# Optimization experiments

Hardware: AMD Instinct MI355X
Metric: run time of the kernel (lower is better)

## Reference

```python
import jax, jax.numpy as jnp
import numpy as np

EPS = 1e-05
HEAD_DIM = 32


def setup_inputs() -> dict:
    key = jax.random.key(0)
    ks = jax.random.split(key, 8)
    b, c, h, w = 8, 512, 64, 64
    s = 1.0 / np.sqrt(c).astype(np.float32)
    return {
        "q": jax.random.normal(ks[0], (b, c, h, w), jnp.float32),
        "k": jax.random.normal(ks[1], (b, c, h, w), jnp.float32),
        "v": jax.random.normal(ks[2], (b, c, h, w), jnp.float32),
        "Wq": jax.random.normal(ks[3], (c, c), jnp.float32) * s,
        "Wk": jax.random.normal(ks[4], (c, c), jnp.float32) * s,
        "Wv": jax.random.normal(ks[5], (c, c), jnp.float32) * s,
        "Wp": jax.random.normal(ks[6], (c, c), jnp.float32) * s,
        "bp": jax.random.normal(ks[7], (c,), jnp.float32) * 0.02,
    }


def reference(q, k, v, Wq, Wk, Wv, Wp, bp):
    b, c, h, w = q.shape
    n = h * w
    hd = HEAD_DIM
    nh = c // hd

    def proj_heads(x, W):
        # NCHW -> (b, n, c) tokens, then Linear (x @ W.T), then split heads
        t = x.reshape(b, c, n).transpose(0, 2, 1)          # (b, n, c)
        y = jnp.einsum('bnc,dc->bnd', t, W)                # torch Linear: x @ W.T
        return y.reshape(b, n, nh, hd)                     # (b, n, h, d)

    # elu feature map: elu(x) + 1
    Q = jax.nn.elu(proj_heads(q, Wq)) + 1.0
    K = jax.nn.elu(proj_heads(k, Wk)) + 1.0
    V = proj_heads(v, Wv)

    # NOTE: faithful to original einsums — KV contracts over HEADS per token,
    # Z uses K summed over the sequence.
    KV = jnp.einsum('bnhd,bnhm->bnmd', K, V)               # (b, n, d_out=m? -> (b,n,hd,hd))
    Z = 1.0 / (jnp.einsum('bnhd,bhd->bnh', Q, K.sum(axis=1)) + EPS)  # (b, n, h)
    out = jnp.einsum('bnhd,bnmd,bnh->bnhm', Q, KV, Z)      # (b, n, h, m)

    out = out.reshape(b, n, c)                             # merge heads
    out = jnp.einsum('bnc,dc->bnd', out, Wp) + bp          # output projection
    return out.transpose(0, 2, 1).reshape(b, c, h, w)
```

## Files before the change

### kernel.cpp

```cpp
#include <hip/hip_runtime.h>
#include <hip/hip_bf16.h>

#define BATCH 8
#define CD 512
#define NT 4096
#define EPSV 1e-5f

using u16x8 = __attribute__((ext_vector_type(8))) unsigned short;
using u16x4 = __attribute__((ext_vector_type(4))) unsigned short;
using bf8   = __attribute__((ext_vector_type(8))) short;
using f32x4 = __attribute__((ext_vector_type(4))) float;

__device__ __forceinline__ float b2f(unsigned short u) {
    union { unsigned int i; float f; } x; x.i = ((unsigned int)u) << 16; return x.f;
}
__device__ __forceinline__ unsigned short f2b(float f) {
    unsigned int x = __float_as_uint(f);
    unsigned int r = (x + 0x7fffu + ((x >> 16) & 1u)) >> 16;
    return (unsigned short)r;
}
__device__ __forceinline__ unsigned int cvtpk(float a, float b) {
    unsigned int r;
    asm("v_cvt_pk_bf16_f32 %0, %1, %2" : "=v"(r) : "v"(a), "v"(b));
    return r;
}
__device__ __forceinline__ void gload_lds16(const void* g, void* l) {
    __builtin_amdgcn_global_load_lds((const __attribute__((address_space(1))) unsigned int*)g,
                                     (__attribute__((address_space(3))) unsigned int*)l, 16, 0, 0);
}
__device__ __forceinline__ int swz8(int r) { return (r ^ (r >> 3)) & 7; }

__global__ __launch_bounds__(256)
void wconv(const float* __restrict__ W0, const float* __restrict__ W1,
           const float* __restrict__ W2, const float* __restrict__ W3,
           unsigned short* __restrict__ Wb) {
    const float* src = (blockIdx.y == 0) ? W0 : (blockIdx.y == 1) ? W1 : (blockIdx.y == 2) ? W2 : W3;
    unsigned short* dst = Wb + (size_t)blockIdx.y * CD * CD;
    const int base = blockIdx.x * 4096 + threadIdx.x * 16;
    u16x8 o0, o1;
    #pragma unroll
    for (int i = 0; i < 4; ++i) {
        float4 v = *reinterpret_cast<const float4*>(src + base + i * 4);
        unsigned short* t = (i < 2) ? (unsigned short*)&o0 : (unsigned short*)&o1;
        t[(i & 1) * 4 + 0] = f2b(v.x); t[(i & 1) * 4 + 1] = f2b(v.y);
        t[(i & 1) * 4 + 2] = f2b(v.z); t[(i & 1) * 4 + 3] = f2b(v.w);
    }
    *(u16x8*)(dst + base)     = o0;
    *(u16x8*)(dst + base + 8) = o1;
}

__global__ __launch_bounds__(256)
void proj_gemm_all(const float* __restrict__ q, const float* __restrict__ k,
                   const float* __restrict__ v, const unsigned short* __restrict__ Wb,
                   unsigned short* __restrict__ Qp, unsigned short* __restrict__ Kp,
                   unsigned short* __restrict__ Vp, float* __restrict__ Kpart) {
    __shared__ __align__(16) unsigned short Xs[64 * 512];
    __shared__ __align__(16) unsigned short Ws[128 * 64];
    const int nper = gridDim.x >> 3;
    const int work = (blockIdx.x & 7) * nper + (blockIdx.x >> 3);
    const int mat  = work / 512;
    const int rem  = work - mat * 512;
    const int b    = rem >> 6;
    const int tile = rem & 63;
    const int n0   = tile * 64;
    const float* Xb = (mat == 0 ? q : mat == 1 ? k : v) + (size_t)b * CD * NT;
    const unsigned short* W = Wb + (size_t)mat * CD * CD;
    unsigned short* Tb = (mat == 0 ? Qp : mat == 1 ? Kp : Vp) + (size_t)b * NT * CD;
    const int act = (mat < 2);

    const int tid = threadIdx.x, lane = tid & 63, wv = tid >> 6;

    #pragma unroll 4
    for (int i = 0; i < 8; ++i) {
        const int s  = i * 256 + tid;
        const int c0 = (s >> 4) * 4;
        const int t0 = (s & 15) * 4;
        const float* p = Xb + (size_t)c0 * NT + n0 + t0;
        float4 r0 = *(const float4*)(p);
        float4 r1 = *(const float4*)(p + NT);
        float4 r2 = *(const float4*)(p + 2 * NT);
        float4 r3 = *(const float4*)(p + 3 * NT);
        float a0[4] = {r0.x, r0.y, r0.z, r0.w};
        float a1[4] = {r1.x, r1.y, r1.z, r1.w};
        float a2[4] = {r2.x, r2.y, r2.z, r2.w};
        float a3[4] = {r3.x, r3.y, r3.z, r3.w};
        #pragma unroll
        for (int j = 0; j < 4; ++j) {
            uint2 u;
            u.x = cvtpk(a0[j], a1[j]);
            u.y = cvtpk(a2[j], a3[j]);
            const int row  = t0 + j;
            const int byte = (row * 1024 + c0 * 2) ^ (swz8(row) << 4);
            *(uint2*)((char*)Xs + byte) = u;
        }
    }
    __syncthreads();

    for (int d0i = 0; d0i < 4; ++d0i) {
        f32x4 acc[4][2];
        #pragma unroll
        for (int m = 0; m < 4; ++m)
            #pragma unroll
            for (int j = 0; j < 2; ++j)
                acc[m][j] = (f32x4){0.f, 0.f, 0.f, 0.f};

        for (int kc = 0; kc < 8; ++kc) {
            #pragma unroll
            for (int it = 0; it < 4; ++it) {
                const int idx = it * 256 + tid;
                const int r = idx >> 3, p = idx & 7;
                gload_lds16(W + (size_t)(d0i * 128 + r) * CD + kc * 64 + (p ^ swz8(r)) * 8,
                            (char*)Ws + idx * 16);
            }
            __syncthreads();
            #pragma unroll
            for (int kk = 0; kk < 2; ++kk) {
                const int kp = kk * 4 + (lane >> 4);
                bf8 af[4], bfr[2];
                #pragma unroll
                for (int m = 0; m < 4; ++m) {
                    const int r = m * 16 + (lane & 15);
                    af[m] = *(const bf8*)((const char*)Xs +
                            ((r * 1024 + kc * 128 + kp * 16) ^ (swz8(r) << 4)));
                }
                #pragma unroll
                for (int j = 0; j < 2; ++j) {
                    const int rw = wv * 32 + j * 16 + (lane & 15);
                    bfr[j] = *(const bf8*)((const char*)Ws + rw * 128 + ((kp ^ swz8(rw)) * 16));
                }
                #pragma unroll
                for (int m = 0; m < 4; ++m)
                    #pragma unroll
                    for (int j = 0; j < 2; ++j)
                        acc[m][j] = __builtin_amdgcn_mfma_f32_16x16x32_bf16(af[m], bfr[j], acc[m][j], 0, 0, 0);
            }
            __syncthreads();
        }

        float kacc[2] = {0.f, 0.f};
        #pragma unroll
        for (int m = 0; m < 4; ++m) {
            const int ib = n0 + m * 16 + ((lane >> 4) << 2);
            #pragma unroll
            for (int j = 0; j < 2; ++j) {
                const int jb = d0i * 128 + wv * 32 + j * 16 + (lane & 15);
                f32x4 vv = acc[m][j];
                #pragma unroll
                for (int r = 0; r < 4; ++r) {
                    float val = vv[r];
                    if (act) val = (val > 0.f) ? (val + 1.f) : __expf(val);
                    if (mat == 1) kacc[j] += val;
                    Tb[(size_t)(ib + r) * CD + jb] = f2b(val);
                }
            }
        }
        if (mat == 1) {
            #pragma unroll
            for (int j = 0; j < 2; ++j) {
                float s = kacc[j];
                s += __shfl_xor(s, 16, 64);
                s += __shfl_xor(s, 32, 64);
                if (lane < 16) {
                    const int jb = d0i * 128 + wv * 32 + j * 16 + lane;
                    Kpart[(size_t)(b * 64 + tile) * CD + jb] = s;
                }
            }
        }
    }
}

__global__ __launch_bounds__(512)
void ksum_red2(const float* __restrict__ Kpart, float* __restrict__ Ks) {
    const int b = blockIdx.x, c = threadIdx.x;
    float s = 0.f;
    #pragma unroll 8
    for (int t = 0; t < 64; ++t) s += Kpart[(size_t)(b * 64 + t) * CD + c];
    Ks[b * CD + c] = s;
}

__global__ __launch_bounds__(256)
void gemm_final(const unsigned short* __restrict__ Wp, const unsigned short* __restrict__ Tm,
                float* __restrict__ out, const float* __restrict__ bias) {
    __shared__ __align__(16) unsigned short Asm[128 * 64];
    __shared__ __align__(16) unsigned short Bsm[128 * 64];
    const int nper = gridDim.x >> 3;
    const int work = (blockIdx.x & 7) * nper + (blockIdx.x >> 3);
    const int i0 = (work & 3) * 128;
    const int j0 = ((work >> 2) & 31) * 128;
    const int b  = work >> 7;
    const unsigned short* Bb = Tm + (size_t)b * NT * CD;
    const int tid  = threadIdx.x;
    const int lane = tid & 63;
    const int wv   = tid >> 6;
    const int wi = wv >> 1, wj = wv & 1;

    f32x4 acc[4][4];
    #pragma unroll
    for (int m = 0; m < 4; ++m)
        #pragma unroll
        for (int j = 0; j < 4; ++j)
            acc[m][j] = (f32x4){0.f, 0.f, 0.f, 0.f};

    for (int k0 = 0; k0 < CD; k0 += 64) {
        #pragma unroll
        for (int it = 0; it < 4; ++it) {
            const int idx = it * 256 + tid;
            const int r = idx >> 3, p = idx & 7;
            const int ps = p ^ (r & 7);
            gload_lds16(Wp + (size_t)(i0 + r) * CD + k0 + ps * 8, (char*)Asm + idx * 16);
            gload_lds16(Bb + (size_t)(j0 + r) * CD + k0 + ps * 8, (char*)Bsm + idx * 16);
        }
        __syncthreads();
        #pragma unroll
        for (int kk = 0; kk < 2; ++kk) {
            bf8 af[4], bfr[4];
            #pragma unroll
            for (int m = 0; m < 4; ++m) {
                const int r  = wi * 64 + m * 16 + (lane & 15);
                const int kp = kk * 4 + (lane >> 4);
                af[m] = *(const bf8*)((const char*)Asm + r * 128 + ((kp ^ (r & 7)) * 16));
            }
            #pragma unroll
            for (int j = 0; j < 4; ++j) {
                const int r  = wj * 64 + j * 16 + (lane & 15);
                const int kp = kk * 4 + (lane >> 4);
                bfr[j] = *(const bf8*)((const char*)Bsm + r * 128 + ((kp ^ (r & 7)) * 16));
            }
            #pragma unroll
            for (int m = 0; m < 4; ++m)
                #pragma unroll
                for (int j = 0; j < 4; ++j)
                    acc[m][j] = __builtin_amdgcn_mfma_f32_16x16x32_bf16(af[m], bfr[j], acc[m][j], 0, 0, 0);
        }
        __syncthreads();
    }

    #pragma unroll
    for (int m = 0; m < 4; ++m) {
        const int ib = i0 + wi * 64 + m * 16 + (lane >> 4) * 4;
        #pragma unroll
        for (int j = 0; j < 4; ++j) {
            const int jb = j0 + wj * 64 + j * 16 + (lane & 15);
            f32x4 v = acc[m][j];
            #pragma unroll
            for (int r = 0; r < 4; ++r)
                out[(size_t)b * CD * NT + (size_t)(ib + r) * NT + jb] = v[r] + bias[ib + r];
        }
    }
}

__global__ __launch_bounds__(256)
void middle2(const unsigned short* __restrict__ Q, const unsigned short* __restrict__ K,
             const unsigned short* __restrict__ V, const float* __restrict__ Ksum,
             unsigned short* __restrict__ T) {
    __shared__ __align__(16) unsigned short sV[4][512];
    __shared__ __align__(16) unsigned short sP[4][16][32];
    const int b = blockIdx.y;
    const int tid = threadIdx.x;
    const int w = tid >> 6, lane = tid & 63;
    const int r16 = lane & 15, g = lane >> 4;
    const int n0 = blockIdx.x * 16 + w * 4;
    const unsigned short* Qb = Q + ((size_t)b * NT + n0) * CD;
    const unsigned short* Kb = K + ((size_t)b * NT + n0) * CD;
    const unsigned short* Vb = V + ((size_t)b * NT + n0) * CD;
    unsigned short* Tb = T + ((size_t)b * NT + n0) * CD;
    const int fragoff = r16 * 32 + g * 8;

    {
        const int r = lane >> 2, cq = lane & 3;
        *(u16x4*)&sP[w][r][16 + cq * 4] = (u16x4){0, 0, 0, 0};
    }

    const float* ksp = Ksum + b * CD + fragoff;
    float ks[8];
    {
        float4 a0 = *(const float4*)ksp;
        float4 a1 = *(const float4*)(ksp + 4);
        ks[0] = a0.x; ks[1] = a0.y; ks[2] = a0.z; ks[3] = a0.w;
        ks[4] = a1.x; ks[5] = a1.y; ks[6] = a1.z; ks[7] = a1.w;
    }
    unsigned short* sVw = &sV[w][0];

    for (int t = 0; t < 4; ++t) {
        asm volatile("s_waitcnt lgkmcnt(0)" ::: "memory");
        __builtin_amdgcn_sched_barrier(0);
        gload_lds16(Vb + (size_t)t * CD + lane * 8, (char*)sVw + lane * 16);

        const bf8 qf = *(const bf8*)(Qb + (size_t)t * CD + fragoff);
        const bf8 kf = *(const bf8*)(Kb + (size_t)t * CD + fragoff);

        f32x4 s = {0.f, 0.f, 0.f, 0.f};
        s = __builtin_amdgcn_mfma_f32_16x16x32_bf16(kf, qf, s, 0, 0, 0);

        float part = 0.f;
        #pragma unroll
        for (int e = 0; e < 8; ++e) part += b2f((unsigned short)qf[e]) * ks[e];
        part += __shfl_xor(part, 16, 64);
        part += __shfl_xor(part, 32, 64);
        const float z = 1.f / (part + EPSV);

        u16x4 pw;
        #pragma unroll
        for (int r = 0; r < 4; ++r) pw[r] = f2b(s[r] * z);
        *(u16x4*)&sP[w][r16][g * 4] = pw;

        asm volatile("s_waitcnt vmcnt(0) lgkmcnt(0)" ::: "memory");
        __builtin_amdgcn_sched_barrier(0);

        const bf8 pb = *(const bf8*)&sP[w][r16][g * 8];
        bf8 va0 = {}, va1 = {};
        if (g < 2) {
            #pragma unroll
            for (int e = 0; e < 8; ++e) {
                va0[e] = (short)sVw[(g * 8 + e) * 32 + r16];
                va1[e] = (short)sVw[(g * 8 + e) * 32 + 16 + r16];
            }
        }

        f32x4 o0 = {0.f, 0.f, 0.f, 0.f}, o1 = {0.f, 0.f, 0.f, 0.f};
        o0 = __builtin_amdgcn_mfma_f32_16x16x32_bf16(va0, pb, o0, 0, 0, 0);
        o1 = __builtin_amdgcn_mfma_f32_16x16x32_bf16(va1, pb, o1, 0, 0, 0);

        u16x4 w0, w1;
        #pragma unroll
        for (int r = 0; r < 4; ++r) { w0[r] = f2b(o0[r]); w1[r] = f2b(o1[r]); }
        *(u16x4*)(Tb + (size_t)t * CD + r16 * 32 + g * 4)      = w0;
        *(u16x4*)(Tb + (size_t)t * CD + r16 * 32 + 16 + g * 4) = w1;
    }
}

extern "C" void kernel_launch(void* const* d_in, const int* in_sizes, int n_in,
                              void* d_out, int out_size, void* d_ws, size_t ws_size,
                              hipStream_t stream) {
    const float* q  = (const float*)d_in[0];
    const float* k  = (const float*)d_in[1];
    const float* v  = (const float*)d_in[2];
    const float* Wq = (const float*)d_in[3];
    const float* Wk = (const float*)d_in[4];
    const float* Wv = (const float*)d_in[5];
    const float* Wp = (const float*)d_in[6];
    const float* bp = (const float*)d_in[7];
    float* out = (float*)d_out;

    const size_t slab = (size_t)BATCH * NT * CD;
    unsigned short* Qp = (unsigned short*)d_ws;
    unsigned short* Kp = Qp + slab;
    unsigned short* Vp = Kp + slab;
    unsigned short* Tm = Vp + slab;
    unsigned short* Wb = Tm + slab;
    float* Kpart = (float*)(Wb + 4 * (size_t)CD * CD);
    float* Ks    = Kpart + (size_t)512 * CD;

    wconv<<<dim3(64, 4), 256, 0, stream>>>(Wq, Wk, Wv, Wp, Wb);

    const unsigned short* Wpb = Wb + (size_t)3 * CD * CD;

    proj_gemm_all<<<1536, 256, 0, stream>>>(q, k, v, Wb, Qp, Kp, Vp, Kpart);

    ksum_red2<<<8, 512, 0, stream>>>(Kpart, Ks);

    middle2<<<dim3(256, 8), 256, 0, stream>>>(Qp, Kp, Vp, Ks, Tm);

    gemm_final<<<1024, 256, 0, stream>>>(Wpb, Tm, out, bp);
}
```

Baseline: 193.7 us.

## Load projection weight fragments directly into registers with double buffering

Drops the LDS staging buffer for weight tiles in the projection GEMM. Each lane now loads its B-operand fragments straight from global memory into registers, double-buffered across k-chunks. This removes the two __syncthreads per k-chunk and the LDS round trip for weights. In exchange it uses more registers and issues global loads that are less coalesced, relying on L2 to serve the weight matrix reused across blocks.

```diff
diff --git a/kernel.cpp b/kernel.cpp
--- a/kernel.cpp
+++ b/kernel.cpp
@@ -49,13 +49,33 @@
     *(u16x8*)(dst + base + 8) = o1;
 }
 
+#define LOADW(WF, KC) do {                                                       \
+    _Pragma("unroll") for (int kk_ = 0; kk_ < 2; ++kk_)                          \
+    _Pragma("unroll") for (int j_ = 0; j_ < 2; ++j_)                             \
+        WF[kk_][j_] = *(const bf8*)(Wd + (size_t)(j_ * 16) * CD + (KC) * 64 + kk_ * 32); \
+} while (0)
+
+#define COMP(WF, KC) do {                                                        \
+    _Pragma("unroll") for (int kk_ = 0; kk_ < 2; ++kk_) {                        \
+        const int kp_ = kk_ * 4 + g;                                             \
+        bf8 af_[4];                                                              \
+        _Pragma("unroll") for (int m_ = 0; m_ < 4; ++m_) {                       \
+            const int r_ = m_ * 16 + r16;                                        \
+            af_[m_] = *(const bf8*)((const char*)Xs +                            \
+                      ((r_ * 1024 + (KC) * 128 + kp_ * 16) ^ (swz8(r_) << 4)));  \
+        }                                                                        \
+        _Pragma("unroll") for (int m_ = 0; m_ < 4; ++m_)                         \
+        _Pragma("unroll") for (int j_ = 0; j_ < 2; ++j_)                         \
+            acc[m_][j_] = __builtin_amdgcn_mfma_f32_16x16x32_bf16(af_[m_], WF[kk_][j_], acc[m_][j_], 0, 0, 0); \
+    }                                                                            \
+} while (0)
+
 __global__ __launch_bounds__(256)
 void proj_gemm_all(const float* __restrict__ q, const float* __restrict__ k,
                    const float* __restrict__ v, const unsigned short* __restrict__ Wb,
                    unsigned short* __restrict__ Qp, unsigned short* __restrict__ Kp,
                    unsigned short* __restrict__ Vp, float* __restrict__ Kpart) {
     __shared__ __align__(16) unsigned short Xs[64 * 512];
-    __shared__ __align__(16) unsigned short Ws[128 * 64];
     const int nper = gridDim.x >> 3;
     const int work = (blockIdx.x & 7) * nper + (blockIdx.x >> 3);
     const int mat  = work / 512;
@@ -69,6 +89,7 @@
     const int act = (mat < 2);
 
     const int tid = threadIdx.x, lane = tid & 63, wv = tid >> 6;
+    const int r16 = lane & 15, g = lane >> 4;
 
     #pragma unroll 4
     for (int i = 0; i < 8; ++i) {
@@ -97,6 +118,7 @@
     __syncthreads();
 
     for (int d0i = 0; d0i < 4; ++d0i) {
+        const unsigned short* Wd = W + (size_t)(d0i * 128 + wv * 32 + r16) * CD + g * 8;
         f32x4 acc[4][2];
         #pragma unroll
         for (int m = 0; m < 4; ++m)
@@ -104,46 +126,23 @@
             for (int j = 0; j < 2; ++j)
                 acc[m][j] = (f32x4){0.f, 0.f, 0.f, 0.f};
 
-        for (int kc = 0; kc < 8; ++kc) {
-            #pragma unroll
-            for (int it = 0; it < 4; ++it) {
-                const int idx = it * 256 + tid;
-                const int r = idx >> 3, p = idx & 7;
-                gload_lds16(W + (size_t)(d0i * 128 + r) * CD + kc * 64 + (p ^ swz8(r)) * 8,
-                            (char*)Ws + idx * 16);
-            }
-            __syncthreads();
-            #pragma unroll
-            for (int kk = 0; kk < 2; ++kk) {
-                const int kp = kk * 4 + (lane >> 4);
-                bf8 af[4], bfr[2];
-                #pragma unroll
-                for (int m = 0; m < 4; ++m) {
-                    const int r = m * 16 + (lane & 15);
-                    af[m] = *(const bf8*)((const char*)Xs +
-                            ((r * 1024 + kc * 128 + kp * 16) ^ (swz8(r) << 4)));
-                }
-                #pragma unroll
-                for (int j = 0; j < 2; ++j) {
-                    const int rw = wv * 32 + j * 16 + (lane & 15);
-                    bfr[j] = *(const bf8*)((const char*)Ws + rw * 128 + ((kp ^ swz8(rw)) * 16));
-                }
-                #pragma unroll
-                for (int m = 0; m < 4; ++m)
-                    #pragma unroll
-                    for (int j = 0; j < 2; ++j)
-                        acc[m][j] = __builtin_amdgcn_mfma_f32_16x16x32_bf16(af[m], bfr[j], acc[m][j], 0, 0, 0);
-            }
-            __syncthreads();
+        bf8 wfA[2][2], wfB[2][2];
+        LOADW(wfA, 0);
+        #pragma unroll
+        for (int kc = 0; kc < 8; kc += 2) {
+            LOADW(wfB, kc + 1);
+            COMP(wfA, kc);
+            if (kc < 6) LOADW(wfA, kc + 2);
+            COMP(wfB, kc + 1);
         }
 
         float kacc[2] = {0.f, 0.f};
         #pragma unroll
         for (int m = 0; m < 4; ++m) {
-            const int ib = n0 + m * 16 + ((lane >> 4) << 2);
+            const int ib = n0 + m * 16 + (g << 2);
             #pragma unroll
             for (int j = 0; j < 2; ++j) {
-                const int jb = d0i * 128 + wv * 32 + j * 16 + (lane & 15);
+                const int jb = d0i * 128 + wv * 32 + j * 16 + r16;
                 f32x4 vv = acc[m][j];
                 #pragma unroll
                 for (int r = 0; r < 4; ++r) {
```

Result: slower. 317.3 us (+63.8%).

## Double-buffer per-wave weight slices in projection GEMM and drop block barriers

Applied to the files above, without the earlier changes.

Reworks the projection GEMM's K loop so each wave loads only its own 32 weight rows into a private, double-buffered LDS slice. The next K-chunk is prefetched while the current one is multiplied, and completion is tracked with explicit vmcnt waits instead of two __syncthreads per chunk. Chunks are now 32 wide (16 iterations) rather than 64 wide (8 iterations), which means more loop iterations and correctness that depends on hand-placed waitcnt and scheduling barriers.

```diff
diff --git a/kernel.cpp b/kernel.cpp
--- a/kernel.cpp
+++ b/kernel.cpp
@@ -55,7 +55,7 @@
                    unsigned short* __restrict__ Qp, unsigned short* __restrict__ Kp,
                    unsigned short* __restrict__ Vp, float* __restrict__ Kpart) {
     __shared__ __align__(16) unsigned short Xs[64 * 512];
-    __shared__ __align__(16) unsigned short Ws[128 * 64];
+    __shared__ __align__(16) unsigned short Wsb[2][128 * 32];
     const int nper = gridDim.x >> 3;
     const int work = (blockIdx.x & 7) * nper + (blockIdx.x >> 3);
     const int mat  = work / 512;
@@ -69,6 +69,7 @@
     const int act = (mat < 2);
 
     const int tid = threadIdx.x, lane = tid & 63, wv = tid >> 6;
+    const int r16 = lane & 15, g = lane >> 4;
 
     #pragma unroll 4
     for (int i = 0; i < 8; ++i) {
@@ -96,6 +97,17 @@
     }
     __syncthreads();
 
+    const int rl0 = lane >> 2;
+    const int sl  = lane & 3;
+    #define ISSUEW(D0I, KC, BUF) do {                                              \
+        _Pragma("unroll") for (int it_ = 0; it_ < 2; ++it_) {                      \
+            const int rl_ = it_ * 16 + rl0;                                        \
+            const int q_  = sl ^ ((rl_ >> 1) & 3);                                 \
+            gload_lds16(W + (size_t)((D0I) * 128 + wv * 32 + rl_) * CD + (KC) * 32 + q_ * 8, \
+                        (char*)Wsb + (BUF) * 8192 + wv * 2048 + it_ * 1024 + lane * 16); \
+        }                                                                          \
+    } while (0)
+
     for (int d0i = 0; d0i < 4; ++d0i) {
         f32x4 acc[4][2];
         #pragma unroll
@@ -104,46 +116,45 @@
             for (int j = 0; j < 2; ++j)
                 acc[m][j] = (f32x4){0.f, 0.f, 0.f, 0.f};
 
-        for (int kc = 0; kc < 8; ++kc) {
-            #pragma unroll
-            for (int it = 0; it < 4; ++it) {
-                const int idx = it * 256 + tid;
-                const int r = idx >> 3, p = idx & 7;
-                gload_lds16(W + (size_t)(d0i * 128 + r) * CD + kc * 64 + (p ^ swz8(r)) * 8,
-                            (char*)Ws + idx * 16);
-            }
-            __syncthreads();
-            #pragma unroll
-            for (int kk = 0; kk < 2; ++kk) {
-                const int kp = kk * 4 + (lane >> 4);
-                bf8 af[4], bfr[2];
+        __builtin_amdgcn_sched_barrier(0);
+        ISSUEW(d0i, 0, 0);
+        __builtin_amdgcn_sched_barrier(0);
+
+        for (int kc = 0; kc < 16; ++kc) {
+            __builtin_amdgcn_sched_barrier(0);
+            if (kc < 15) ISSUEW(d0i, kc + 1, (kc + 1) & 1);
+            __builtin_amdgcn_sched_barrier(0);
+            if (kc < 15) asm volatile("s_waitcnt vmcnt(2)" ::: "memory");
+            else         asm volatile("s_waitcnt vmcnt(0)" ::: "memory");
+            __builtin_amdgcn_sched_barrier(0);
+
+            const char* Wcur = (const char*)Wsb + (kc & 1) * 8192 + wv * 2048;
+            bf8 af[4], bfr[2];
+            #pragma unroll
+            for (int m = 0; m < 4; ++m) {
+                const int r = m * 16 + r16;
+                af[m] = *(const bf8*)((const char*)Xs +
+                        ((r * 1024 + kc * 64 + g * 16) ^ (swz8(r) << 4)));
+            }
+            #pragma unroll
+            for (int j = 0; j < 2; ++j) {
+                const int lr = j * 16 + r16;
+                bfr[j] = *(const bf8*)(Wcur + lr * 64 + ((g ^ ((lr >> 1) & 3)) * 16));
+            }
+            #pragma unroll
+            for (int m = 0; m < 4; ++m)
                 #pragma unroll
-                for (int m = 0; m < 4; ++m) {
-                    const int r = m * 16 + (lane & 15);
-                    af[m] = *(const bf8*)((const char*)Xs +
-                            ((r * 1024 + kc * 128 + kp * 16) ^ (swz8(r) << 4)));
-                }
-                #pragma unroll
-                for (int j = 0; j < 2; ++j) {
-                    const int rw = wv * 32 + j * 16 + (lane & 15);
-                    bfr[j] = *(const bf8*)((const char*)Ws + rw * 128 + ((kp ^ swz8(rw)) * 16));
-                }
-                #pragma unroll
-                for (int m = 0; m < 4; ++m)
-                    #pragma unroll
-                    for (int j = 0; j < 2; ++j)
-                        acc[m][j] = __builtin_amdgcn_mfma_f32_16x16x32_bf16(af[m], bfr[j], acc[m][j], 0, 0, 0);
-            }
-            __syncthreads();
+                for (int j = 0; j < 2; ++j)
+                    acc[m][j] = __builtin_amdgcn_mfma_f32_16x16x32_bf16(af[m], bfr[j], acc[m][j], 0, 0, 0);
         }
 
         float kacc[2] = {0.f, 0.f};
         #pragma unroll
         for (int m = 0; m < 4; ++m) {
-            const int ib = n0 + m * 16 + ((lane >> 4) << 2);
+            const int ib = n0 + m * 16 + (g << 2);
             #pragma unroll
             for (int j = 0; j < 2; ++j) {
-                const int jb = d0i * 128 + wv * 32 + j * 16 + (lane & 15);
+                const int jb = d0i * 128 + wv * 32 + j * 16 + r16;
                 f32x4 vv = acc[m][j];
                 #pragma unroll
                 for (int r = 0; r < 4; ++r) {
@@ -167,6 +178,7 @@
             }
         }
     }
+    #undef ISSUEW
 }
 
 __global__ __launch_bounds__(512)
```

After: 177.1 us. 1.09x faster.

## Split projection into transpose-convert pass plus 128x128 tiled bf16 GEMMs

Applied to the files above, without the earlier changes.

Replaces the fused projection kernel, which loaded a 64-token fp32 tile, transposed it into LDS and streamed W per 128-column chunk. A separate kernel now transposes and converts q/k/v to token-major bf16 in workspace, and three templated GEMMs with 128x128 tiles load both operands via global_load_lds. This gives more MFMA reuse per LDS load and a more regular GEMM, but adds a full extra write and read of the bf16 activations plus more launches. Workspace slabs are rotated so the outputs fit in the existing buffers.

```diff
diff --git a/kernel.cpp b/kernel.cpp
--- a/kernel.cpp
+++ b/kernel.cpp
@@ -28,7 +28,6 @@
     __builtin_amdgcn_global_load_lds((const __attribute__((address_space(1))) unsigned int*)g,
                                      (__attribute__((address_space(3))) unsigned int*)l, 16, 0, 0);
 }
-__device__ __forceinline__ int swz8(int r) { return (r ^ (r >> 3)) & 7; }
 
 __global__ __launch_bounds__(256)
 void wconv(const float* __restrict__ W0, const float* __restrict__ W1,
@@ -50,32 +49,27 @@
 }
 
 __global__ __launch_bounds__(256)
-void proj_gemm_all(const float* __restrict__ q, const float* __restrict__ k,
-                   const float* __restrict__ v, const unsigned short* __restrict__ Wb,
-                   unsigned short* __restrict__ Qp, unsigned short* __restrict__ Kp,
-                   unsigned short* __restrict__ Vp, float* __restrict__ Kpart) {
-    __shared__ __align__(16) unsigned short Xs[64 * 512];
-    __shared__ __align__(16) unsigned short Ws[128 * 64];
-    const int nper = gridDim.x >> 3;
-    const int work = (blockIdx.x & 7) * nper + (blockIdx.x >> 3);
-    const int mat  = work / 512;
-    const int rem  = work - mat * 512;
-    const int b    = rem >> 6;
-    const int tile = rem & 63;
-    const int n0   = tile * 64;
+void tconvA(const float* __restrict__ q, const float* __restrict__ k, const float* __restrict__ v,
+            unsigned short* __restrict__ Qt, unsigned short* __restrict__ Kt,
+            unsigned short* __restrict__ Vt) {
+    __shared__ __align__(16) unsigned short T[32 * 520];
+    const int bid = blockIdx.x;
+    const int mat = bid >> 10;
+    const int rem = bid & 1023;
+    const int b   = rem >> 7;
+    const int nt  = rem & 127;
+    const int n0  = nt * 32;
     const float* Xb = (mat == 0 ? q : mat == 1 ? k : v) + (size_t)b * CD * NT;
-    const unsigned short* W = Wb + (size_t)mat * CD * CD;
-    unsigned short* Tb = (mat == 0 ? Qp : mat == 1 ? Kp : Vp) + (size_t)b * NT * CD;
-    const int act = (mat < 2);
-
-    const int tid = threadIdx.x, lane = tid & 63, wv = tid >> 6;
-
-    #pragma unroll 4
-    for (int i = 0; i < 8; ++i) {
+    unsigned short* Yb = (mat == 0 ? Qt : mat == 1 ? Kt : Vt) + (size_t)b * NT * CD;
+    const int tid = threadIdx.x;
+
+    #pragma unroll
+    for (int i = 0; i < 4; ++i) {
         const int s  = i * 256 + tid;
-        const int c0 = (s >> 4) * 4;
-        const int t0 = (s & 15) * 4;
-        const float* p = Xb + (size_t)c0 * NT + n0 + t0;
+        const int tq = s & 7;
+        const int cq = s >> 3;
+        const int c0 = cq * 4;
+        const float* p = Xb + (size_t)c0 * NT + n0 + tq * 4;
         float4 r0 = *(const float4*)(p);
         float4 r1 = *(const float4*)(p + NT);
         float4 r2 = *(const float4*)(p + 2 * NT);
@@ -89,81 +83,109 @@
             uint2 u;
             u.x = cvtpk(a0[j], a1[j]);
             u.y = cvtpk(a2[j], a3[j]);
-            const int row  = t0 + j;
-            const int byte = (row * 1024 + c0 * 2) ^ (swz8(row) << 4);
-            *(uint2*)((char*)Xs + byte) = u;
+            const int row = tq * 4 + j;
+            const int xr  = (row >> 2) & 3;
+            const int byte = row * 1040 + (((cq >> 1) ^ xr) << 4) + ((cq & 1) << 3);
+            *(uint2*)((char*)T + byte) = u;
         }
     }
     __syncthreads();
 
-    for (int d0i = 0; d0i < 4; ++d0i) {
-        f32x4 acc[4][2];
-        #pragma unroll
-        for (int m = 0; m < 4; ++m)
-            #pragma unroll
-            for (int j = 0; j < 2; ++j)
-                acc[m][j] = (f32x4){0.f, 0.f, 0.f, 0.f};
-
-        for (int kc = 0; kc < 8; ++kc) {
-            #pragma unroll
-            for (int it = 0; it < 4; ++it) {
-                const int idx = it * 256 + tid;
-                const int r = idx >> 3, p = idx & 7;
-                gload_lds16(W + (size_t)(d0i * 128 + r) * CD + kc * 64 + (p ^ swz8(r)) * 8,
-                            (char*)Ws + idx * 16);
-            }
-            __syncthreads();
-            #pragma unroll
-            for (int kk = 0; kk < 2; ++kk) {
+    const int row = tid >> 3;
+    const int xr  = (row >> 2) & 3;
+    #pragma unroll
+    for (int p2 = 0; p2 < 8; ++p2) {
+        const int cs = (tid & 7) + p2 * 8;
+        u16x8 val = *(const u16x8*)((const char*)T + row * 1040 + ((cs ^ xr) << 4));
+        *(u16x8*)(Yb + (size_t)(n0 + row) * CD + cs * 8) = val;
+    }
+}
+
+template<int ACT, int KSUM>
+__global__ __launch_bounds__(256)
+void proj_gemm(const unsigned short* __restrict__ A, const unsigned short* __restrict__ W,
+               unsigned short* __restrict__ Out, float* __restrict__ Kpart) {
+    __shared__ __align__(16) unsigned short Asm[128 * 64];
+    __shared__ __align__(16) unsigned short Bsm[128 * 64];
+    const int nper = gridDim.x >> 3;
+    const int work = (blockIdx.x & 7) * nper + (blockIdx.x >> 3);
+    const int d0 = (work & 3) * 128;
+    const int ti = (work >> 2) & 31;
+    const int i0 = ti * 128;
+    const int b  = work >> 7;
+    const unsigned short* Ab = A + (size_t)b * NT * CD;
+    unsigned short* Ob = Out + (size_t)b * NT * CD;
+    const int tid  = threadIdx.x;
+    const int lane = tid & 63;
+    const int wv   = tid >> 6;
+    const int wi = wv >> 1, wj = wv & 1;
+
+    f32x4 acc[4][4];
+    #pragma unroll
+    for (int m = 0; m < 4; ++m)
+        #pragma unroll
+        for (int j = 0; j < 4; ++j)
+            acc[m][j] = (f32x4){0.f, 0.f, 0.f, 0.f};
+
+    for (int k0 = 0; k0 < CD; k0 += 64) {
+        #pragma unroll
+        for (int it = 0; it < 4; ++it) {
+            const int idx = it * 256 + tid;
+            const int r = idx >> 3, p = idx & 7;
+            const int ps = p ^ (r & 7);
+            gload_lds16(Ab + (size_t)(i0 + r) * CD + k0 + ps * 8, (char*)Asm + idx * 16);
+            gload_lds16(W  + (size_t)(d0 + r) * CD + k0 + ps * 8, (char*)Bsm + idx * 16);
+        }
+        __syncthreads();
+        #pragma unroll
+        for (int kk = 0; kk < 2; ++kk) {
+            bf8 af[4], bfr[4];
+            #pragma unroll
+            for (int m = 0; m < 4; ++m) {
+                const int r  = wi * 64 + m * 16 + (lane & 15);
                 const int kp = kk * 4 + (lane >> 4);
-                bf8 af[4], bfr[2];
+                af[m] = *(const bf8*)((const char*)Asm + r * 128 + ((kp ^ (r & 7)) * 16));
+            }
+            #pragma unroll
+            for (int j = 0; j < 4; ++j) {
+                const int r  = wj * 64 + j * 16 + (lane & 15);
+                const int kp = kk * 4 + (lane >> 4);
+                bfr[j] = *(const bf8*)((const char*)Bsm + r * 128 + ((kp ^ (r & 7)) * 16));
+            }
+            #pragma unroll
+            for (int m = 0; m < 4; ++m)
                 #pragma unroll
-                for (int m = 0; m < 4; ++m) {
-                    const int r = m * 16 + (lane & 15);
-                    af[m] = *(const bf8*)((const char*)Xs +
-                            ((r * 1024 + kc * 128 + kp * 16) ^ (swz8(r) << 4)));
-                }
-                #pragma unroll
-                for (int j = 0; j < 2; ++j) {
-                    const int rw = wv * 32 + j * 16 + (lane & 15);
-                    bfr[j] = *(const bf8*)((const char*)Ws + rw * 128 + ((kp ^ swz8(rw)) * 16));
-                }
-                #pragma unroll
-                for (int m = 0; m < 4; ++m)
-                    #pragma unroll
-                    for (int j = 0; j < 2; ++j)
-                        acc[m][j] = __builtin_amdgcn_mfma_f32_16x16x32_bf16(af[m], bfr[j], acc[m][j], 0, 0, 0);
-            }
-            __syncthreads();
-        }
-
-        float kacc[2] = {0.f, 0.f};
-        #pragma unroll
-        for (int m = 0; m < 4; ++m) {
-            const int ib = n0 + m * 16 + ((lane >> 4) << 2);
-            #pragma unroll
-            for (int j = 0; j < 2; ++j) {
-                const int jb = d0i * 128 + wv * 32 + j * 16 + (lane & 15);
-                f32x4 vv = acc[m][j];
-                #pragma unroll
-                for (int r = 0; r < 4; ++r) {
-                    float val = vv[r];
-                    if (act) val = (val > 0.f) ? (val + 1.f) : __expf(val);
-                    if (mat == 1) kacc[j] += val;
-                    Tb[(size_t)(ib + r) * CD + jb] = f2b(val);
-                }
-            }
-        }
-        if (mat == 1) {
-            #pragma unroll
-            for (int j = 0; j < 2; ++j) {
-                float s = kacc[j];
-                s += __shfl_xor(s, 16, 64);
-                s += __shfl_xor(s, 32, 64);
-                if (lane < 16) {
-                    const int jb = d0i * 128 + wv * 32 + j * 16 + lane;
-                    Kpart[(size_t)(b * 64 + tile) * CD + jb] = s;
-                }
+                for (int j = 0; j < 4; ++j)
+                    acc[m][j] = __builtin_amdgcn_mfma_f32_16x16x32_bf16(af[m], bfr[j], acc[m][j], 0, 0, 0);
+        }
+        __syncthreads();
+    }
+
+    float kacc[4] = {0.f, 0.f, 0.f, 0.f};
+    #pragma unroll
+    for (int m = 0; m < 4; ++m) {
+        const int ib = i0 + wi * 64 + m * 16 + (lane >> 4) * 4;
+        #pragma unroll
+        for (int j = 0; j < 4; ++j) {
+            const int jb = d0 + wj * 64 + j * 16 + (lane & 15);
+            f32x4 vv = acc[m][j];
+            #pragma unroll
+            for (int r = 0; r < 4; ++r) {
+                float val = vv[r];
+                if (ACT) val = (val > 0.f) ? (val + 1.f) : __expf(val);
+                if (KSUM) kacc[j] += val;
+                Ob[(size_t)(ib + r) * CD + jb] = f2b(val);
+            }
+        }
+    }
+    if (KSUM) {
+        #pragma unroll
+        for (int j = 0; j < 4; ++j) {
+            float s = kacc[j];
+            s += __shfl_xor(s, 16, 64);
+            s += __shfl_xor(s, 32, 64);
+            if (lane < 16) {
+                Kpart[(size_t)(b * 64 + ti * 2 + wi) * CD + d0 + wj * 64 + j * 16 + lane] = s;
             }
         }
     }
@@ -343,23 +365,30 @@
     float* out = (float*)d_out;
 
     const size_t slab = (size_t)BATCH * NT * CD;
-    unsigned short* Qp = (unsigned short*)d_ws;
-    unsigned short* Kp = Qp + slab;
-    unsigned short* Vp = Kp + slab;
-    unsigned short* Tm = Vp + slab;
-    unsigned short* Wb = Tm + slab;
+    unsigned short* S0 = (unsigned short*)d_ws;
+    unsigned short* S1 = S0 + slab;
+    unsigned short* S2 = S1 + slab;
+    unsigned short* S3 = S2 + slab;
+    unsigned short* Wb = S3 + slab;
     float* Kpart = (float*)(Wb + 4 * (size_t)CD * CD);
-    float* Ks    = Kpart + (size_t)512 * CD;
+    float* Ks    = Kpart + (size_t)BATCH * 64 * CD;
 
     wconv<<<dim3(64, 4), 256, 0, stream>>>(Wq, Wk, Wv, Wp, Wb);
 
+    const unsigned short* Wqb = Wb;
+    const unsigned short* Wkb = Wb + (size_t)CD * CD;
+    const unsigned short* Wvb = Wb + (size_t)2 * CD * CD;
     const unsigned short* Wpb = Wb + (size_t)3 * CD * CD;
 
-    proj_gemm_all<<<1536, 256, 0, stream>>>(q, k, v, Wb, Qp, Kp, Vp, Kpart);
+    tconvA<<<3072, 256, 0, stream>>>(q, k, v, S0, S1, S2);
+
+    proj_gemm<1, 0><<<1024, 256, 0, stream>>>(S0, Wqb, S3, nullptr);
+    proj_gemm<1, 1><<<1024, 256, 0, stream>>>(S1, Wkb, S0, Kpart);
+    proj_gemm<0, 0><<<1024, 256, 0, stream>>>(S2, Wvb, S1, nullptr);
 
     ksum_red2<<<8, 512, 0, stream>>>(Kpart, Ks);
 
-    middle2<<<dim3(256, 8), 256, 0, stream>>>(Qp, Kp, Vp, Ks, Tm);
-
-    gemm_final<<<1024, 256, 0, stream>>>(Wpb, Tm, out, bp);
-}
+    middle2<<<dim3(256, 8), 256, 0, stream>>>(S3, S0, S1, Ks, S2);
+
+    gemm_final<<<1024, 256, 0, stream>>>(Wpb, S2, out, bp);
+}
```

New measurement: 211.7 us. 9.3% more time.
